# Optimization experiments

Measured on AMD Instinct MI355X. Metric: run time of the kernel, lower is better.

The kernel has to match this reference:

```python
import jax, jax.numpy as jnp
import numpy as np
from jax import lax

THRESHOLD = 0.25
DECAY = 0.9
STRIDE = 1
PADDING = 1


def setup_inputs() -> dict:
    key = jax.random.key(0)
    k1, k2 = jax.random.split(key)
    # binary spike train: (B, C_in, H, W, T)
    x = (jax.random.uniform(k1, (8, 16, 64, 64, 32)) < 0.2).astype(jnp.float32)
    # conv weight: (C_out, C_in, k, k), init ~ randn * 0.1 as in the torch module
    weight = jax.random.normal(k2, (32, 16, 3, 3), dtype=jnp.float32) * 0.1
    return {"x": x, "weight": weight}


def _conv(xt, weight):
    # xt: (B, C_in, H, W) -> (B, C_out, H_out, W_out)
    return lax.conv_general_dilated(
        xt, weight,
        window_strides=(STRIDE, STRIDE),
        padding=[(PADDING, PADDING), (PADDING, PADDING)],
        dimension_numbers=("NCHW", "OIHW", "NCHW"),
    )


def reference(x, weight):
    B, Cin, H, W, T = x.shape
    Cout, k = weight.shape[0], weight.shape[2]
    Hout = (H + 2 * PADDING - k) // STRIDE + 1
    Wout = (W + 2 * PADDING - k) // STRIDE + 1

    xt = jnp.moveaxis(x, -1, 0)  # (T, B, Cin, H, W)
    mem0 = jnp.zeros((B, Cout, Hout, Wout), dtype=jnp.float32)

    def step(mem, x_t):
        # accumulate conv activation, then decay (order matches original: += then *=)
        mem = (mem + _conv(x_t, weight)) * DECAY
        spike = (mem >= THRESHOLD).astype(mem.dtype)
        mem = mem * (1.0 - spike)  # reset fired neurons to 0
        return mem, spike

    _, spikes = lax.scan(step, mem0, xt)  # spikes: (T, B, Cout, Hout, Wout)
    return jnp.moveaxis(spikes, 0, -1)    # (B, Cout, Hout, Wout, T)
```

## Files before the change

### kernel.cpp

```cpp
#include <hip/hip_runtime.h>


#define BB   8
#define CIN  16
#define HH   64
#define WW   64
#define TT   32
#define COUT 32
#define HWT  (HH * WW * TT)

typedef float f32x2 __attribute__((ext_vector_type(2)));

__global__ void repack_w(const float* __restrict__ wgt, float* __restrict__ wT) {
    const int e = blockIdx.x * 256 + threadIdx.x;
    if (e < 144 * 32) {
        const int co  = e & 31;
        const int tau = e >> 5;
        const int ci  = tau & 15;
        const int khw = tau >> 4;
        wT[tau * 32 + co] = wgt[co * 144 + ci * 9 + khw];
    }
}

__global__ __launch_bounds__(256, 6)
void snn_main(const float* __restrict__ x, const float* __restrict__ wT,
              float* __restrict__ out) {
    const int wk = (blockIdx.x & 7) * 512 + (blockIdx.x >> 3);
    const int b  = wk >> 9;
    const int h  = (wk >> 3) & 63;
    const int w0 = (wk & 7) * 8;

    const int tid = threadIdx.x;
    const int t   = tid & 31;
    const int wi  = tid >> 5;
    const int w   = w0 + wi;

    f32x2 acc2[16];
#pragma unroll
    for (int i = 0; i < 16; ++i) acc2[i] = (f32x2){0.0f, 0.0f};

#pragma unroll
    for (int kh = 0; kh < 3; ++kh) {
        const int hs = h + kh - 1;
        if ((unsigned)hs >= HH) continue;
#pragma unroll
        for (int kw = 0; kw < 3; ++kw) {
            const int ws  = w + kw - 1;
            const bool ok = (unsigned)ws < WW;
            const int wsc = ok ? ws : 0;
            const float* xp  = x + ((b * CIN * HH + hs) * WW + wsc) * TT + t;
            const f32x2* wr2 = (const f32x2*)(wT + (kh * 3 + kw) * (CIN * 32));
#pragma unroll
            for (int ci = 0; ci < CIN; ++ci) {
                float xv = xp[ci * HWT];
                xv = ok ? xv : 0.0f;
                const f32x2 xv2 = {xv, xv};
#pragma unroll
                for (int c2 = 0; c2 < 16; ++c2)
                    acc2[c2] = __builtin_elementwise_fma(xv2, wr2[ci * 16 + c2],
                                                         acc2[c2]);
            }
        }
    }

    __shared__ float s_tr[128 * 36];
#pragma unroll
    for (int p = 0; p < 2; ++p) {
        if (p) __syncthreads();
#pragma unroll
        for (int j = 0; j < 16; ++j) {
            const int c = 16 * p + j;
            s_tr[(j * 8 + wi) * 36 + t] = acc2[c >> 1][c & 1];
        }
        __syncthreads();
        if (tid < 128) {
            const int j2  = tid >> 3;
            const int wi2 = tid & 7;
            const int co2 = 16 * p + j2;
            const float* rr = s_tr + tid * 36;
            float* op = out + (((b * COUT + co2) * HH + h) * WW + (w0 + wi2)) * TT;
            float mem = 0.0f;
#pragma unroll
            for (int t4 = 0; t4 < TT; t4 += 4) {
                const float4 q = *reinterpret_cast<const float4*>(rr + t4);
                const float cv[4] = {q.x, q.y, q.z, q.w};
                float4 o;
                float* vp = &o.x;
#pragma unroll
                for (int jj = 0; jj < 4; ++jj) {
                    mem = (mem + cv[jj]) * 0.9f;
                    const bool sp = (mem >= 0.25f);
                    vp[jj] = sp ? 1.0f : 0.0f;
                    if (sp) mem = 0.0f;
                }
                *reinterpret_cast<float4*>(op + t4) = o;
            }
        }
    }
}

extern "C" void kernel_launch(void* const* d_in, const int* in_sizes, int n_in,
                              void* d_out, int out_size, void* d_ws, size_t ws_size,
                              hipStream_t stream) {
    const float* x   = (const float*)d_in[0];
    const float* wgt = (const float*)d_in[1];
    float* out = (float*)d_out;
    float* wT  = (float*)d_ws;

    repack_w<<<18, 256, 0, stream>>>(wgt, wT);

    snn_main<<<dim3(4096), dim3(256), 0, stream>>>(x, wT, out);
}
```

Before: 264.8 us.

## Software-pipeline conv tap loads with double-buffered registers and inline packed FMA

Unrolls the nine 3x3 taps and issues loads for the next tap into a second register buffer while FMAs run on the current one, so global-load latency overlaps compute. The FMA is written as inline v_pk_fma_f32 asm with the weight forced to a scalar operand, and the row-boundary check becomes a select instead of a skip. Occupancy hint drops from 6 to 4 blocks per CU to leave room for the extra registers. This trades occupancy-based latency hiding for explicit prefetch, and the asm 's' constraint may add scalar moves.

```diff
diff --git a/kernel.cpp b/kernel.cpp
--- a/kernel.cpp
+++ b/kernel.cpp
@@ -22,7 +22,40 @@
     }
 }
 
-__global__ __launch_bounds__(256, 6)
+#define LOADTAP(M, XV)                                                      \
+    {                                                                       \
+        const int kh = (M) / 3, kw = (M) % 3;                               \
+        const int hs = h + kh - 1;                                          \
+        const int ws = w + kw - 1;                                          \
+        const bool okh = (unsigned)hs < HH;                                 \
+        const bool okw = (unsigned)ws < WW;                                 \
+        const int hsc = okh ? hs : 0;                                       \
+        const int wsc = okw ? ws : 0;                                       \
+        const float* xp = x + ((b * CIN * HH + hsc) * WW + wsc) * TT + t;   \
+        _Pragma("unroll")                                                   \
+        for (int ci = 0; ci < CIN; ++ci) XV[ci] = xp[ci * HWT];             \
+        const bool ok = okh && okw;                                         \
+        _Pragma("unroll")                                                   \
+        for (int ci = 0; ci < CIN; ++ci) XV[ci] = ok ? XV[ci] : 0.0f;       \
+    }
+
+#define FMATAP(M, XV)                                                       \
+    {                                                                       \
+        const f32x2* wr2 = (const f32x2*)(wT + (M) * (CIN * 32));           \
+        _Pragma("unroll")                                                   \
+        for (int ci = 0; ci < CIN; ++ci) {                                  \
+            const f32x2 xv2 = {XV[ci], XV[ci]};                             \
+            _Pragma("unroll")                                               \
+            for (int c2 = 0; c2 < 16; ++c2) {                               \
+                const f32x2 wv = wr2[ci * 16 + c2];                         \
+                asm("v_pk_fma_f32 %0, %1, %2, %0"                           \
+                    : "+v"(acc2[c2])                                        \
+                    : "v"(xv2), "s"(wv));                                   \
+            }                                                               \
+        }                                                                   \
+    }
+
+__global__ __launch_bounds__(256, 4)
 void snn_main(const float* __restrict__ x, const float* __restrict__ wT,
               float* __restrict__ out) {
     const int wk = (blockIdx.x & 7) * 512 + (blockIdx.x >> 3);
@@ -39,29 +72,18 @@
 #pragma unroll
     for (int i = 0; i < 16; ++i) acc2[i] = (f32x2){0.0f, 0.0f};
 
-#pragma unroll
-    for (int kh = 0; kh < 3; ++kh) {
-        const int hs = h + kh - 1;
-        if ((unsigned)hs >= HH) continue;
-#pragma unroll
-        for (int kw = 0; kw < 3; ++kw) {
-            const int ws  = w + kw - 1;
-            const bool ok = (unsigned)ws < WW;
-            const int wsc = ok ? ws : 0;
-            const float* xp  = x + ((b * CIN * HH + hs) * WW + wsc) * TT + t;
-            const f32x2* wr2 = (const f32x2*)(wT + (kh * 3 + kw) * (CIN * 32));
-#pragma unroll
-            for (int ci = 0; ci < CIN; ++ci) {
-                float xv = xp[ci * HWT];
-                xv = ok ? xv : 0.0f;
-                const f32x2 xv2 = {xv, xv};
-#pragma unroll
-                for (int c2 = 0; c2 < 16; ++c2)
-                    acc2[c2] = __builtin_elementwise_fma(xv2, wr2[ci * 16 + c2],
-                                                         acc2[c2]);
-            }
-        }
-    }
+    float xv0[16], xv1[16];
+
+    LOADTAP(0, xv0)
+    LOADTAP(1, xv1)  FMATAP(0, xv0)
+    LOADTAP(2, xv0)  FMATAP(1, xv1)
+    LOADTAP(3, xv1)  FMATAP(2, xv0)
+    LOADTAP(4, xv0)  FMATAP(3, xv1)
+    LOADTAP(5, xv1)  FMATAP(4, xv0)
+    LOADTAP(6, xv0)  FMATAP(5, xv1)
+    LOADTAP(7, xv1)  FMATAP(6, xv0)
+    LOADTAP(8, xv0)  FMATAP(7, xv1)
+                     FMATAP(8, xv0)
 
     __shared__ float s_tr[128 * 36];
 #pragma unroll
```

New measurement: 319.0 us. 20.5% more time.
